# Kernel optimization log

Measured on AMD Instinct MI355X. Metric: run time of the kernel, lower is better.

## Reference

```python
import jax, jax.numpy as jnp
import numpy as np
from jax import lax

B, C, H, W = 4, 64, 96, 96
K = 9  # 3x3 kernel taps


def setup_inputs() -> dict:
    key = jax.random.key(0)
    k1, k2, k3 = jax.random.split(key, 3)
    x = jax.random.normal(k1, (B, C, H, W), dtype=jnp.float32)
    # offset conv: small init so predicted offsets are modest (deform conv convention)
    w_off = jax.random.normal(k2, (18, C, 3, 3), dtype=jnp.float32) * 0.01
    b_off = jnp.zeros((18,), dtype=jnp.float32)
    # main deformable conv weights (fan-in scaled)
    w_dc = jax.random.normal(k3, (C, C, 3, 3), dtype=jnp.float32) * (1.0 / np.sqrt(C * 9))
    b_dc = jnp.zeros((C,), dtype=jnp.float32)
    return {"x": x, "w_off": w_off, "b_off": b_off, "w_dc": w_dc, "b_dc": b_dc}


def _deform_conv(x, offset, w_dc, b_dc):
    # x: [B,C,H,W]; offset: [B,2K,H,W] laid out as (dy,dx) per tap, row-major taps
    b, c, h, w = x.shape
    off = offset.reshape(b, K, 2, h, w)
    ky, kx = jnp.meshgrid(jnp.arange(3), jnp.arange(3), indexing="ij")
    ky = ky.reshape(K).astype(x.dtype)  # tap row offsets 0..2
    kx = kx.reshape(K).astype(x.dtype)
    hh = jnp.arange(h, dtype=x.dtype)[None, None, :, None]
    ww = jnp.arange(w, dtype=x.dtype)[None, None, None, :]
    pad = 1.0
    # absolute sampling coordinates [B,K,H,W]
    py = hh + (ky - pad)[None, :, None, None] + off[:, :, 0]
    px = ww + (kx - pad)[None, :, None, None] + off[:, :, 1]

    y0 = jnp.floor(py)
    x0 = jnp.floor(px)
    ly = (py - y0)[:, None]  # [B,1,K,H,W]
    lx = (px - x0)[:, None]
    y0i = y0.astype(jnp.int32)
    x0i = x0.astype(jnp.int32)

    x_flat = x.reshape(b, c, h * w)

    def gather(yi, xi):
        valid = (yi >= 0) & (yi < h) & (xi >= 0) & (xi < w)
        yc = jnp.clip(yi, 0, h - 1)
        xc = jnp.clip(xi, 0, w - 1)
        idx = (yc * w + xc).reshape(b, 1, K * h * w)
        v = jnp.take_along_axis(x_flat, idx, axis=2).reshape(b, c, K, h, w)
        return v * valid.astype(x.dtype)[:, None]  # zero padding outside image

    v00 = gather(y0i, x0i)
    v01 = gather(y0i, x0i + 1)
    v10 = gather(y0i + 1, x0i)
    v11 = gather(y0i + 1, x0i + 1)
    samp = (v00 * (1 - ly) * (1 - lx) + v01 * (1 - ly) * lx
            + v10 * ly * (1 - lx) + v11 * ly * lx)  # [B,C,K,H,W]

    out = jnp.einsum("bckhw,ock->bohw", samp, w_dc.reshape(c, c, K))
    return out + b_dc[None, :, None, None]


def reference(x, w_off, b_off, w_dc, b_dc):
    offset = lax.conv_general_dilated(
        x, w_off, window_strides=(1, 1), padding=((1, 1), (1, 1)),
        dimension_numbers=("NCHW", "OIHW", "NCHW"))
    offset = offset + b_off[None, :, None, None]
    return _deform_conv(x, offset, w_dc, b_dc)
```

## Files before the change

### kernel.cpp

```cpp
#include <hip/hip_runtime.h>
#include <math.h>

typedef _Float16 h4    __attribute__((ext_vector_type(4)));
typedef _Float16 half8 __attribute__((ext_vector_type(8)));
typedef float    f32x4 __attribute__((ext_vector_type(4)));

constexpr int B = 4, C = 64, H = 96, W = 96;
constexpr int NQ = C / 4;
constexpr int KT = 9, OFFC = 18;
constexpr int HW = H * W;
constexpr int PAD = 4;
constexpr int HP = H + 2 * PAD, WP = W + 2 * PAD;
constexpr int HPWP = HP * WP;
constexpr int WDF_HALFS = 4 * KT * 2 * 64 * 8;
constexpr int WOF_HALFS = 2 * KT * 2 * 64 * 8;

struct h4x2 { h4 a, b; };

__global__ __launch_bounds__(256) void prep(
        const float* __restrict__ x, const float* __restrict__ w_off,
        const float* __restrict__ w_dc,
        h4* __restrict__ xpad4, _Float16* __restrict__ wdf,
        _Float16* __restrict__ wof) {
    const int i = blockIdx.x * 256 + threadIdx.x;
    {
        int col = i % WP; int t = i / WP; int row = t % HP; int bq = t / HP;
        int b = bq / NQ, q = bq % NQ;
        int h = row - PAD, w = col - PAD;
        h4 v; v[0] = v[1] = v[2] = v[3] = (_Float16)0.f;
        if (h >= 0 && h < H && w >= 0 && w < W) {
            const float* xp = x + ((size_t)b * C + 4 * q) * HW + h * W + w;
            v[0] = (_Float16)xp[0];
            v[1] = (_Float16)xp[HW];
            v[2] = (_Float16)xp[2 * HW];
            v[3] = (_Float16)xp[3 * HW];
        }
        xpad4[i] = v;
    }
    if (i < WDF_HALFS) {
        int m = i / 9216, r = i % 9216;
        int tap = r / 1024, l = (r >> 3) & 63, j = i & 7;
        int ks = (r >> 9) & 1;
        int o = m * 16 + (l & 15);
        int c = ks * 32 + ((l >> 4) << 3) + j;
        wdf[i] = (_Float16)w_dc[((size_t)o * C + c) * KT + tap];
    }
    if (i < WOF_HALFS) {
        int mf = i / 9216, r = i % 9216;
        int tap = r / 1024, l = (r >> 3) & 63, j = i & 7;
        int ks = (r >> 9) & 1;
        int oc = mf * 16 + (l & 15);
        int c = ks * 32 + ((l >> 4) << 3) + j;
        wof[i] = (oc < OFFC) ? (_Float16)w_off[((size_t)oc * C + c) * KT + tap]
                             : (_Float16)0.f;
    }
}

__global__ __launch_bounds__(256, 2) void fused_wave(
        const h4* __restrict__ xpad4, const _Float16* __restrict__ wdf,
        const _Float16* __restrict__ wof, const float* __restrict__ b_off,
        const float* __restrict__ b_dc, float* __restrict__ out) {
    const int lane = threadIdx.x & 63;
    const int wid = __builtin_amdgcn_readfirstlane(threadIdx.x >> 6);
    const int p = lane & 15, g = lane >> 4;
    const int bid = blockIdx.x;
    const int tile = (bid & 7) * 72 + (bid >> 3);
    const int wt = tile * 4 + wid;
    const int flat0 = wt * 16;
    const int b_u = __builtin_amdgcn_readfirstlane(flat0 / HW);
    const int loc0 = flat0 - b_u * HW;
    const int h = loc0 / W;
    const int w = loc0 % W + p;

    __shared__ _Float16 wlds[WDF_HALFS];
    __shared__ float offt[4][2 * KT][16];

    const h4* xq = xpad4 + (size_t)b_u * NQ * HPWP;

    {
        f32x4 a0 = {0.f,0.f,0.f,0.f}, a1 = {0.f,0.f,0.f,0.f};
        half8 bf[3][2];
        half8 wA[2][4];
        const _Float16* wofb = wof + lane * 8;

        auto loadWA = [&](int slot, int k) {
            #pragma unroll
            for (int ks = 0; ks < 2; ++ks) {
                wA[slot][2 * ks]     = *(const half8*)(wofb + k * 1024 + ks * 512);
                wA[slot][2 * ks + 1] = *(const half8*)(wofb + 9216 + k * 1024 + ks * 512);
            }
        };
        auto issueA = [&](int s, int k) {
            const int cell = (h + k / 3 - 1 + PAD) * WP + (w + k % 3 - 1 + PAD);
            #pragma unroll
            for (int ks = 0; ks < 2; ++ks) {
                h4 q0 = xq[(size_t)(ks * 8 + 2 * g)     * HPWP + cell];
                h4 q1 = xq[(size_t)(ks * 8 + 2 * g + 1) * HPWP + cell];
                bf[s][ks] = __builtin_shufflevector(q0, q1, 0,1,2,3,4,5,6,7);
            }
        };
        auto mfmaA = [&](int s, int slot) {
            __builtin_amdgcn_s_setprio(1);
            #pragma unroll
            for (int ks = 0; ks < 2; ++ks) {
                a0 = __builtin_amdgcn_mfma_f32_16x16x32_f16(wA[slot][2*ks],   bf[s][ks], a0, 0, 0, 0);
                a1 = __builtin_amdgcn_mfma_f32_16x16x32_f16(wA[slot][2*ks+1], bf[s][ks], a1, 0, 0, 0);
            }
            __builtin_amdgcn_s_setprio(0);
        };

        loadWA(0, 0); loadWA(1, 1);
        issueA(0, 0); issueA(1, 1); issueA(2, 2);
        #pragma unroll
        for (int k = 1; k <= 8; ++k) {
            __builtin_amdgcn_sched_barrier(0);
            mfmaA((k - 1) % 3, (k - 1) & 1);
            __builtin_amdgcn_sched_barrier(0);
            if (k <= 7) loadWA((k - 1) & 1, k + 1);
            if (k <= 6) issueA((k - 1) % 3, k + 2);
        }

        #pragma unroll
        for (int s2 = 0; s2 < 18; ++s2) {
            const int seg = wid * 18 + s2;
            __builtin_amdgcn_global_load_lds(
                (const __attribute__((address_space(1))) unsigned int*)
                    (wdf + (size_t)seg * 512 + lane * 8),
                (__attribute__((address_space(3))) unsigned int*)
                    &wlds[seg * 512],
                16, 0, 0);
        }
        __builtin_amdgcn_sched_barrier(0);
        mfmaA(8 % 3, 8 & 1);

        #pragma unroll
        for (int r = 0; r < 4; ++r) {
            const int oc = g * 4 + r;
            offt[wid][oc][p] = a0[r] + b_off[oc];
        }
        if (g == 0) {
            #pragma unroll
            for (int r = 0; r < 2; ++r)
                offt[wid][16 + r][p] = a1[r] + b_off[16 + r];
        }
    }
    __syncthreads();

    {
        f32x4 acc[4] = {{0.f,0.f,0.f,0.f},{0.f,0.f,0.f,0.f},
                        {0.f,0.f,0.f,0.f},{0.f,0.f,0.f,0.f}};
        h4x2 rt[3][2][2], rb[3][2][2];
        h4 Wc[3][4];
        const _Float16* wl = wlds + lane * 8;

        auto issueB = [&](int s, int k) {
            const float dy = offt[wid][2 * k][p];
            const float dx = offt[wid][2 * k + 1][p];
            const float py = (float)(h + k / 3 - 1) + dy;
            const float px = (float)(w + k % 3 - 1) + dx;
            const float y0f = floorf(py), x0f = floorf(px);
            const float ly = py - y0f, lx = px - x0f;
            int y0 = (int)y0f, x0 = (int)x0f;
            y0 = min(max(y0, -PAD), H + PAD - 2);
            x0 = min(max(x0, -PAD), W + PAD - 2);
            const int base = (y0 + PAD) * WP + (x0 + PAD);
            const float a11 = ly * lx;
            const _Float16 f11 = (_Float16)a11;
            const _Float16 f10 = (_Float16)(ly - a11);
            const _Float16 f01 = (_Float16)(lx - a11);
            const _Float16 f00 = (_Float16)(1.f - ly - lx + a11);
            #pragma unroll
            for (int e = 0; e < 4; ++e) { Wc[s][0][e] = f00; Wc[s][1][e] = f01;
                                          Wc[s][2][e] = f10; Wc[s][3][e] = f11; }
            #pragma unroll
            for (int ks = 0; ks < 2; ++ks) {
                #pragma unroll
                for (int q2 = 0; q2 < 2; ++q2) {
                    const h4* qp = xq + (size_t)(ks * 8 + 2 * g + q2) * HPWP + base;
                    __builtin_memcpy(&rt[s][ks][q2], qp, 16);
                    __builtin_memcpy(&rb[s][ks][q2], qp + WP, 16);
                }
            }
        };
        auto mfmaB = [&](int s, int k) {
            #pragma unroll
            for (int ks = 0; ks < 2; ++ks) {
                h4 s0 = rt[s][ks][0].a * Wc[s][0] + rt[s][ks][0].b * Wc[s][1]
                      + rb[s][ks][0].a * Wc[s][2] + rb[s][ks][0].b * Wc[s][3];
                h4 s1 = rt[s][ks][1].a * Wc[s][0] + rt[s][ks][1].b * Wc[s][1]
                      + rb[s][ks][1].a * Wc[s][2] + rb[s][ks][1].b * Wc[s][3];
                half8 bfr = __builtin_shufflevector(s0, s1, 0,1,2,3,4,5,6,7);
                __builtin_amdgcn_s_setprio(1);
                #pragma unroll
                for (int m = 0; m < 4; ++m) {
                    half8 wf = *(const half8*)(wl + m * 9216 + k * 1024 + ks * 512);
                    acc[m] = __builtin_amdgcn_mfma_f32_16x16x32_f16(wf, bfr,
                                                                    acc[m], 0, 0, 0);
                }
                __builtin_amdgcn_s_setprio(0);
            }
        };

        issueB(0, 0); issueB(1, 1); issueB(2, 2);
        #pragma unroll
        for (int k = 1; k <= 8; ++k) {
            __builtin_amdgcn_sched_barrier(0);
            mfmaB((k - 1) % 3, k - 1);
            __builtin_amdgcn_sched_barrier(0);
            if (k <= 6) issueB((k - 1) % 3, k + 2);
        }
        mfmaB(8 % 3, 8);

        #pragma unroll
        for (int m = 0; m < 4; ++m) {
            #pragma unroll
            for (int r = 0; r < 4; ++r) {
                const int o = m * 16 + g * 4 + r;
                out[((size_t)b_u * C + o) * HW + loc0 + p] = acc[m][r] + b_dc[o];
            }
        }
    }
}

extern "C" void kernel_launch(void* const* d_in, const int* in_sizes, int n_in,
                              void* d_out, int out_size, void* d_ws, size_t ws_size,
                              hipStream_t stream) {
    const float* x     = (const float*)d_in[0];
    const float* w_off = (const float*)d_in[1];
    const float* b_off = (const float*)d_in[2];
    const float* w_dc  = (const float*)d_in[3];
    const float* b_dc  = (const float*)d_in[4];
    float* out = (float*)d_out;

    char* ws = (char*)d_ws;
    h4*        xpad4 = (h4*)ws;
    _Float16*  wdf   = (_Float16*)(ws + 5537792);
    _Float16*  wof   = (_Float16*)(ws + 5537792 + 73728);

    prep<<<B * NQ * HPWP / 256, 256, 0, stream>>>(x, w_off, w_dc, xpad4, wdf, wof);
    fused_wave<<<576, 256, 0, stream>>>(xpad4, wdf, wof, b_off, b_dc, out);
}
```

Baseline: 30.87 us.

## Use 9-wave blocks over 256 tiles and shrink pipelines to double buffering

Blocks grow from 4 to 9 waves, and the grid shrinks to 256 blocks so each CU handles one block covering 144 pixels. The shared weight copy into LDS is spread over 9 waves (8 segments each), so fewer blocks each load the full weight set. The gather/MFMA software pipeline depth drops from three stages to two, which frees registers to make room for the larger block. The tradeoffs are less latency hiding per wave and possible loss of two-blocks-per-CU occupancy.

```diff
diff --git a/kernel.cpp b/kernel.cpp
--- a/kernel.cpp
+++ b/kernel.cpp
@@ -14,6 +14,7 @@
 constexpr int HPWP = HP * WP;
 constexpr int WDF_HALFS = 4 * KT * 2 * 64 * 8;
 constexpr int WOF_HALFS = 2 * KT * 2 * 64 * 8;
+constexpr int NWAVE = 9;
 
 struct h4x2 { h4 a, b; };
 
@@ -56,7 +57,7 @@
     }
 }
 
-__global__ __launch_bounds__(256, 2) void fused_wave(
+__global__ __launch_bounds__(NWAVE * 64) void fused_wave(
         const h4* __restrict__ xpad4, const _Float16* __restrict__ wdf,
         const _Float16* __restrict__ wof, const float* __restrict__ b_off,
         const float* __restrict__ b_dc, float* __restrict__ out) {
@@ -64,22 +65,21 @@
     const int wid = __builtin_amdgcn_readfirstlane(threadIdx.x >> 6);
     const int p = lane & 15, g = lane >> 4;
     const int bid = blockIdx.x;
-    const int tile = (bid & 7) * 72 + (bid >> 3);
-    const int wt = tile * 4 + wid;
-    const int flat0 = wt * 16;
+    const int tile = (bid & 7) * 32 + (bid >> 3);
+    const int flat0 = tile * 144 + wid * 16;
     const int b_u = __builtin_amdgcn_readfirstlane(flat0 / HW);
     const int loc0 = flat0 - b_u * HW;
     const int h = loc0 / W;
     const int w = loc0 % W + p;
 
     __shared__ _Float16 wlds[WDF_HALFS];
-    __shared__ float offt[4][2 * KT][16];
+    __shared__ float offt[NWAVE][2 * KT][16];
 
     const h4* xq = xpad4 + (size_t)b_u * NQ * HPWP;
 
     {
         f32x4 a0 = {0.f,0.f,0.f,0.f}, a1 = {0.f,0.f,0.f,0.f};
-        half8 bf[3][2];
+        half8 bf[2][2];
         half8 wA[2][4];
         const _Float16* wofb = wof + lane * 8;
 
@@ -110,19 +110,21 @@
         };
 
         loadWA(0, 0); loadWA(1, 1);
-        issueA(0, 0); issueA(1, 1); issueA(2, 2);
+        issueA(0, 0); issueA(1, 1);
         #pragma unroll
         for (int k = 1; k <= 8; ++k) {
             __builtin_amdgcn_sched_barrier(0);
-            mfmaA((k - 1) % 3, (k - 1) & 1);
-            __builtin_amdgcn_sched_barrier(0);
-            if (k <= 7) loadWA((k - 1) & 1, k + 1);
-            if (k <= 6) issueA((k - 1) % 3, k + 2);
-        }
-
-        #pragma unroll
-        for (int s2 = 0; s2 < 18; ++s2) {
-            const int seg = wid * 18 + s2;
+            mfmaA((k - 1) & 1, (k - 1) & 1);
+            __builtin_amdgcn_sched_barrier(0);
+            if (k <= 7) {
+                loadWA((k - 1) & 1, k + 1);
+                issueA((k - 1) & 1, k + 1);
+            }
+        }
+
+        #pragma unroll
+        for (int s2 = 0; s2 < 8; ++s2) {
+            const int seg = wid * 8 + s2;
             __builtin_amdgcn_global_load_lds(
                 (const __attribute__((address_space(1))) unsigned int*)
                     (wdf + (size_t)seg * 512 + lane * 8),
@@ -131,7 +133,7 @@
                 16, 0, 0);
         }
         __builtin_amdgcn_sched_barrier(0);
-        mfmaA(8 % 3, 8 & 1);
+        mfmaA(8 & 1, 8 & 1);
 
         #pragma unroll
         for (int r = 0; r < 4; ++r) {
@@ -149,8 +151,8 @@
     {
         f32x4 acc[4] = {{0.f,0.f,0.f,0.f},{0.f,0.f,0.f,0.f},
                         {0.f,0.f,0.f,0.f},{0.f,0.f,0.f,0.f}};
-        h4x2 rt[3][2][2], rb[3][2][2];
-        h4 Wc[3][4];
+        h4x2 rt[2][2][2], rb[2][2][2];
+        h4 Wc[2][4];
         const _Float16* wl = wlds + lane * 8;
 
         auto issueB = [&](int s, int k) {
@@ -201,15 +203,15 @@
             }
         };
 
-        issueB(0, 0); issueB(1, 1); issueB(2, 2);
+        issueB(0, 0); issueB(1, 1);
         #pragma unroll
         for (int k = 1; k <= 8; ++k) {
             __builtin_amdgcn_sched_barrier(0);
-            mfmaB((k - 1) % 3, k - 1);
-            __builtin_amdgcn_sched_barrier(0);
-            if (k <= 6) issueB((k - 1) % 3, k + 2);
-        }
-        mfmaB(8 % 3, 8);
+            mfmaB((k - 1) & 1, k - 1);
+            __builtin_amdgcn_sched_barrier(0);
+            if (k <= 7) issueB((k - 1) & 1, k + 1);
+        }
+        mfmaB(8 & 1, 8);
 
         #pragma unroll
         for (int m = 0; m < 4; ++m) {
@@ -238,5 +240,5 @@
     _Float16*  wof   = (_Float16*)(ws + 5537792 + 73728);
 
     prep<<<B * NQ * HPWP / 256, 256, 0, stream>>>(x, w_off, w_dc, xpad4, wdf, wof);
-    fused_wave<<<576, 256, 0, stream>>>(xpad4, wdf, wof, b_off, b_dc, out);
+    fused_wave<<<256, NWAVE * 64, 0, stream>>>(xpad4, wdf, wof, b_off, b_dc, out);
 }
```

Measured after the change: 26.48 us. 1.17x faster.
